# Kernel optimization log

Measured on AMD Instinct MI355X. Metric: run time of the kernel, lower is better.

The kernel has to match this reference:

```python
import jax, jax.numpy as jnp
import numpy as np
import math

D, H, DK, F, V, L = 512, 8, 64, 2048, 8192, 2
B, S, T = 16, 128, 128
EPS = 1e-5


def _ln(x, g, b):
    mu = jnp.mean(x, -1, keepdims=True)
    var = jnp.mean((x - mu) ** 2, -1, keepdims=True)
    return g * (x - mu) * jax.lax.rsqrt(var + EPS) + b


def _pe(length):
    pos = jnp.arange(length, dtype=jnp.float32)[:, None]
    div = jnp.exp(jnp.arange(0, D, 2, dtype=jnp.float32) * (-math.log(10000.0) / D))
    ang = pos * div
    pe = jnp.zeros((length, D), jnp.float32)
    return pe.at[:, 0::2].set(jnp.sin(ang)).at[:, 1::2].set(jnp.cos(ang))


def _attn(q, k, v, src, dst, num_dst):
    # per-edge score = exp(clip((k_src . q_dst)/sqrt(d_k), -5, 5))  [E, H]
    score = jnp.einsum('ehd,ehd->eh', k[src], q[dst]) / math.sqrt(DK)
    score = jnp.exp(jnp.clip(score, -5.0, 5.0))
    wv = jax.ops.segment_sum(v[src] * score[..., None], dst, num_segments=num_dst)
    z = jax.ops.segment_sum(score, dst, num_segments=num_dst)
    return (wv / z[..., None]).reshape(num_dst, D)


def _forward(src_tokens, tgt_tokens, ee_src, ee_dst, dd_src, dd_dst, ed_src, ed_dst, P):
    (src_emb, tgt_emb, eW, eB, elg, elb, eW1, eb1, eW2, eb2, eng, enb,
     dsW, dsB, dcW, dcB, dlg, dlb, dW1, db1, dW2, db2, dng, dnb, gW, gb) = P
    pe = _pe(max(S, T))
    Ne, Nd = B * S, B * T
    xe = (src_emb[src_tokens] * math.sqrt(D) + pe[None, :S]).reshape(Ne, D)
    xd = (tgt_emb[tgt_tokens] * math.sqrt(D) + pe[None, :T]).reshape(Nd, D)
    # encoder stack
    for i in range(L):
        nx = _ln(xe, elg[i, 0], elb[i, 0])
        q = (nx @ eW[i, 0] + eB[i, 0]).reshape(Ne, H, DK)
        k = (nx @ eW[i, 1] + eB[i, 1]).reshape(Ne, H, DK)
        v = (nx @ eW[i, 2] + eB[i, 2]).reshape(Ne, H, DK)
        xe = xe + _attn(q, k, v, ee_src, ee_dst, Ne) @ eW[i, 3] + eB[i, 3]
        nx = _ln(xe, elg[i, 1], elb[i, 1])
        xe = xe + jax.nn.relu(nx @ eW1[i] + eb1[i]) @ eW2[i] + eb2[i]
        if i == L - 1:
            xe = _ln(xe, eng, enb)
    # decoder stack
    for i in range(L):
        nx = _ln(xd, dlg[i, 0], dlb[i, 0])
        q = (nx @ dsW[i, 0] + dsB[i, 0]).reshape(Nd, H, DK)
        k = (nx @ dsW[i, 1] + dsB[i, 1]).reshape(Nd, H, DK)
        v = (nx @ dsW[i, 2] + dsB[i, 2]).reshape(Nd, H, DK)
        xd = xd + _attn(q, k, v, dd_src, dd_dst, Nd) @ dsW[i, 3] + dsB[i, 3]
        nq = _ln(xd, dlg[i, 1], dlb[i, 1])
        nkv = _ln(xe, dlg[i, 1], dlb[i, 1])
        q = (nq @ dcW[i, 0] + dcB[i, 0]).reshape(Nd, H, DK)
        k = (nkv @ dcW[i, 1] + dcB[i, 1]).reshape(Ne, H, DK)
        v = (nkv @ dcW[i, 2] + dcB[i, 2]).reshape(Ne, H, DK)
        xd = xd + _attn(q, k, v, ed_src, ed_dst, Nd) @ dcW[i, 3] + dcB[i, 3]
        nx = _ln(xd, dlg[i, 2], dlb[i, 2])
        xd = xd + jax.nn.relu(nx @ dW1[i] + db1[i]) @ dW2[i] + db2[i]
        if i == L - 1:
            xd = _ln(xd, dng, dnb)
    return jax.nn.log_softmax(xd @ gW + gb, axis=-1)  # [Nd, V]


def setup_inputs() -> dict:
    key = jax.random.key(0)
    ks = iter(jax.random.split(key, 40))
    def nrm(shape, scale=0.02):
        return jax.random.normal(next(ks), shape, dtype=jnp.float32) * scale
    src_tokens = jax.random.randint(next(ks), (B, S), 0, V, dtype=jnp.int32)
    tgt_tokens = jax.random.randint(next(ks), (B, T), 0, V, dtype=jnp.int32)
    # graph structure (per-sentence blocks)
    si, di = np.meshgrid(np.arange(S), np.arange(S), indexing='ij')
    si, di = si.ravel(), di.ravel()
    base = (np.arange(B) * S)[:, None]
    ee_src = (base + si[None, :]).ravel().astype(np.int32)
    ee_dst = (base + di[None, :]).ravel().astype(np.int32)
    m = si <= di  # causal: src pos <= dst pos
    dd_src = (base + si[m][None, :]).ravel().astype(np.int32)
    dd_dst = (base + di[m][None, :]).ravel().astype(np.int32)
    ed_src = ee_src.copy()
    ed_dst = ee_dst.copy()
    inp = dict(
        src_tokens=src_tokens, tgt_tokens=tgt_tokens,
        ee_src=jnp.asarray(ee_src), ee_dst=jnp.asarray(ee_dst),
        dd_src=jnp.asarray(dd_src), dd_dst=jnp.asarray(dd_dst),
        ed_src=jnp.asarray(ed_src), ed_dst=jnp.asarray(ed_dst),
        src_emb=nrm((V, D), 1.0 / math.sqrt(D)), tgt_emb=nrm((V, D), 1.0 / math.sqrt(D)),
        enc_attn_W=nrm((L, 4, D, D)), enc_attn_b=jnp.zeros((L, 4, D), jnp.float32),
        enc_ln_g=jnp.ones((L, 2, D), jnp.float32), enc_ln_b=jnp.zeros((L, 2, D), jnp.float32),
        enc_ff_W1=nrm((L, D, F)), enc_ff_b1=jnp.zeros((L, F), jnp.float32),
        enc_ff_W2=nrm((L, F, D)), enc_ff_b2=jnp.zeros((L, D), jnp.float32),
        enc_norm_g=jnp.ones((D,), jnp.float32), enc_norm_b=jnp.zeros((D,), jnp.float32),
        dec_self_W=nrm((L, 4, D, D)), dec_self_b=jnp.zeros((L, 4, D), jnp.float32),
        dec_cross_W=nrm((L, 4, D, D)), dec_cross_b=jnp.zeros((L, 4, D), jnp.float32),
        dec_ln_g=jnp.ones((L, 3, D), jnp.float32), dec_ln_b=jnp.zeros((L, 3, D), jnp.float32),
        dec_ff_W1=nrm((L, D, F)), dec_ff_b1=jnp.zeros((L, F), jnp.float32),
        dec_ff_W2=nrm((L, F, D)), dec_ff_b2=jnp.zeros((L, D), jnp.float32),
        dec_norm_g=jnp.ones((D,), jnp.float32), dec_norm_b=jnp.zeros((D,), jnp.float32),
        gen_W=nrm((D, V)), gen_b=jnp.zeros((V,), jnp.float32),
    )
    return inp


def reference(src_tokens, tgt_tokens, ee_src, ee_dst, dd_src, dd_dst, ed_src, ed_dst,
              src_emb, tgt_emb, enc_attn_W, enc_attn_b, enc_ln_g, enc_ln_b,
              enc_ff_W1, enc_ff_b1, enc_ff_W2, enc_ff_b2, enc_norm_g, enc_norm_b,
              dec_self_W, dec_self_b, dec_cross_W, dec_cross_b, dec_ln_g, dec_ln_b,
              dec_ff_W1, dec_ff_b1, dec_ff_W2, dec_ff_b2, dec_norm_g, dec_norm_b,
              gen_W, gen_b):
    P = (src_emb, tgt_emb, enc_attn_W, enc_attn_b, enc_ln_g, enc_ln_b,
         enc_ff_W1, enc_ff_b1, enc_ff_W2, enc_ff_b2, enc_norm_g, enc_norm_b,
         dec_self_W, dec_self_b, dec_cross_W, dec_cross_b, dec_ln_g, dec_ln_b,
         dec_ff_W1, dec_ff_b1, dec_ff_W2, dec_ff_b2, dec_norm_g, dec_norm_b, gen_W, gen_b)
    return _forward(src_tokens, tgt_tokens, ee_src, ee_dst, dd_src, dd_dst, ed_src, ed_dst, P)
```

## Files before the change

kernel.cpp:

```cpp
#include <hip/hip_runtime.h>

typedef __attribute__((ext_vector_type(8))) short bfx8;
typedef __attribute__((ext_vector_type(4))) float fx4;

static __device__ __forceinline__ unsigned short f2bf(float f) {
    union { float f; unsigned int u; } v; v.f = f;
    unsigned int i = v.u;
    return (unsigned short)((i + 0x7FFFu + ((i >> 16) & 1u)) >> 16);
}
static __device__ __forceinline__ float bf2f(unsigned short u) {
    union { unsigned int ui; float f; } cv;
    cv.ui = ((unsigned int)u) << 16;
    return cv.f;
}

static __device__ __forceinline__ void gl2lds16(const unsigned short* g, unsigned short* l) {
    unsigned long long gu = (unsigned long long)g;
    unsigned int lu = (unsigned int)(unsigned long long)l;
    __builtin_amdgcn_global_load_lds(
        (const __attribute__((address_space(1))) void*)gu,
        (__attribute__((address_space(3))) void*)lu,
        16, 0, 0);
}

struct TrGroup {
    const float* src;
    unsigned short* dst;
    int srcRowStride;
    int dstRowStride;
    long srcSliceOff;
    long dstSliceOff;
};
struct TrTable {
    TrGroup g[18];
    int zStart[19];
};

__global__ __launch_bounds__(256) void trall_kernel(TrTable tt)
{
    __shared__ unsigned short tile[32][33];
    int z = blockIdx.z;
    int gi = 0;
#pragma unroll 1
    while (z >= tt.zStart[gi + 1]) ++gi;
    int zi = z - tt.zStart[gi];
    const float* s = tt.g[gi].src + (size_t)zi * tt.g[gi].srcSliceOff;
    unsigned short* d = tt.g[gi].dst + (size_t)zi * tt.g[gi].dstSliceOff;
    int srs = tt.g[gi].srcRowStride, drs = tt.g[gi].dstRowStride;
    int n0 = blockIdx.x * 32, k0 = blockIdx.y * 32;
    int tx = threadIdx.x & 31, ty = threadIdx.x >> 5;
#pragma unroll
    for (int i = 0; i < 32; i += 8)
        tile[ty + i][tx] = f2bf(s[(size_t)(k0 + ty + i) * srs + (n0 + tx)]);
    __syncthreads();
#pragma unroll
    for (int i = 0; i < 32; i += 8)
        d[(size_t)(n0 + ty + i) * drs + (k0 + tx)] = tile[tx][ty + i];
}

__global__ __launch_bounds__(256) void embed2_kernel(
    const int* __restrict__ tokA, const int* __restrict__ tokB,
    const float* __restrict__ embA, const float* __restrict__ embB,
    float* __restrict__ outA, float* __restrict__ outB)
{
    int idx = blockIdx.x;
    int row = idx & 2047;
    const int* tok = idx < 2048 ? tokA : tokB;
    const float* emb = idx < 2048 ? embA : embB;
    float* out = idx < 2048 ? outA : outB;
    int pos = row & 127;
    int t = tok[row];
    for (int d = threadIdx.x; d < 512; d += 256) {
        float ang = (float)pos * expf((float)(d & ~1) * (-9.210340371976184f / 512.0f));
        float pe = (d & 1) ? cosf(ang) : sinf(ang);
        out[(size_t)row * 512 + d] = emb[(size_t)t * 512 + d] * 22.627416997969522f + pe;
    }
}

static __device__ __forceinline__ void ln_row(
    const float* __restrict__ xrow, const float* __restrict__ g,
    const float* __restrict__ b, int lane, fx4& o0, fx4& o1)
{
    const fx4* xr = (const fx4*)xrow;
    fx4 a = xr[lane * 2], c = xr[lane * 2 + 1];
    float s = a[0] + a[1] + a[2] + a[3] + c[0] + c[1] + c[2] + c[3];
#pragma unroll
    for (int off = 32; off; off >>= 1) s += __shfl_xor(s, off);
    float mu = s * (1.0f / 512.0f);
    float qv = 0.f;
#pragma unroll
    for (int j = 0; j < 4; ++j) {
        float d0 = a[j] - mu; qv += d0 * d0;
        float d1 = c[j] - mu; qv += d1 * d1;
    }
#pragma unroll
    for (int off = 32; off; off >>= 1) qv += __shfl_xor(qv, off);
    float rs = rsqrtf(qv * (1.0f / 512.0f) + 1e-5f);
    const fx4* gr = (const fx4*)g;
    const fx4* br = (const fx4*)b;
    fx4 g0 = gr[lane * 2], g1 = gr[lane * 2 + 1];
    fx4 b0 = br[lane * 2], b1 = br[lane * 2 + 1];
#pragma unroll
    for (int j = 0; j < 4; ++j) {
        o0[j] = g0[j] * (a[j] - mu) * rs + b0[j];
        o1[j] = g1[j] * (c[j] - mu) * rs + b1[j];
    }
}

template<bool OUTBF>
__global__ __launch_bounds__(256) void ln_kernel(
    const float* __restrict__ x, const float* __restrict__ g,
    const float* __restrict__ b, void* __restrict__ out)
{
    int row = blockIdx.x * 4 + (threadIdx.x >> 6);
    int lane = threadIdx.x & 63;
    fx4 o0, o1;
    ln_row(x + (size_t)row * 512, g, b, lane, o0, o1);
    if (OUTBF) {
        unsigned short* orow = (unsigned short*)out + (size_t)row * 512 + lane * 8;
        ushort4 u0 = {f2bf(o0[0]), f2bf(o0[1]), f2bf(o0[2]), f2bf(o0[3])};
        ushort4 u1 = {f2bf(o1[0]), f2bf(o1[1]), f2bf(o1[2]), f2bf(o1[3])};
        *(ushort4*)orow = u0;
        *(ushort4*)(orow + 4) = u1;
    } else {
        fx4* orow = (fx4*)out + (size_t)row * 128;
        orow[lane * 2] = o0;
        orow[lane * 2 + 1] = o1;
    }
}

__global__ __launch_bounds__(256) void ln2_kernel(
    const float* __restrict__ x0, const float* __restrict__ x1,
    const float* __restrict__ g, const float* __restrict__ b,
    unsigned short* __restrict__ o0, unsigned short* __restrict__ o1)
{
    int idx = blockIdx.x * 4 + (threadIdx.x >> 6);
    int lane = threadIdx.x & 63;
    const float* x = idx < 2048 ? x0 : x1;
    unsigned short* o = idx < 2048 ? o0 : o1;
    int row = idx & 2047;
    fx4 v0, v1;
    ln_row(x + (size_t)row * 512, g, b, lane, v0, v1);
    unsigned short* orow = o + (size_t)row * 512 + lane * 8;
    ushort4 u0 = {f2bf(v0[0]), f2bf(v0[1]), f2bf(v0[2]), f2bf(v0[3])};
    ushort4 u1 = {f2bf(v1[0]), f2bf(v1[1]), f2bf(v1[2]), f2bf(v1[3])};
    *(ushort4*)orow = u0;
    *(ushort4*)(orow + 4) = u1;
}

template<bool RELU, bool RESID, bool OUTBF>
__global__ __launch_bounds__(256) void gemm_kernel(
    const unsigned short* __restrict__ A, const unsigned short* __restrict__ Wt,
    const float* __restrict__ bias, const float* __restrict__ res,
    void* __restrict__ Cv, int K, int ldc, int gx)
{
    __shared__ unsigned short smem[2][2][4096];
    const int tid = threadIdx.x;
    const int nwg = gridDim.x;
    const int cpx = nwg >> 3;
    const int phys = blockIdx.x;
    const int logical = (phys & 7) * cpx + (phys >> 3);
    const int bm = (logical / gx) * 64;
    const int bn = (logical % gx) * 64;
    const int lane = tid & 63;
    const int wv = tid >> 6;
    const int wr = (wv >> 1) * 32;
    const int wc = (wv & 1) * 32;
    const int lr = lane & 15;
    const int lrow = lane >> 3;
    const int lchk = lane & 7;
    fx4 acc00 = {0.f, 0.f, 0.f, 0.f}, acc01 = {0.f, 0.f, 0.f, 0.f};
    fx4 acc10 = {0.f, 0.f, 0.f, 0.f}, acc11 = {0.f, 0.f, 0.f, 0.f};

    auto stage = [&](int buf, int k0) {
#pragma unroll
        for (int j = 0; j < 2; ++j) {
            int row = wv * 16 + j * 8 + lrow;
            int sc = lchk ^ (row & 7);
            gl2lds16(A + (size_t)(bm + row) * K + k0 + sc * 8,
                     &smem[buf][0][(wv * 16 + j * 8) * 64]);
        }
#pragma unroll
        for (int j = 0; j < 2; ++j) {
            int row = wv * 16 + j * 8 + lrow;
            int sc = lchk ^ (row & 7);
            gl2lds16(Wt + (size_t)(bn + row) * K + k0 + sc * 8,
                     &smem[buf][1][(wv * 16 + j * 8) * 64]);
        }
    };

    const int nt = K >> 6;
    int cur = 0;
    stage(0, 0);
    for (int t = 0; t < nt; ++t) {
        __syncthreads();
        if (t + 1 < nt) stage(cur ^ 1, (t + 1) << 6);
        const unsigned short* bufA = &smem[cur][0][0];
        const unsigned short* bufB = &smem[cur][1][0];
        const int ra0 = wr + lr, ra1 = wr + 16 + lr;
        const int rb0 = wc + lr, rb1 = wc + 16 + lr;
#pragma unroll
        for (int kk = 0; kk < 2; ++kk) {
            int ca = kk * 4 + (lane >> 4);
            bfx8 a0 = *(const bfx8*)&bufA[ra0 * 64 + ((ca ^ (ra0 & 7)) * 8)];
            bfx8 a1 = *(const bfx8*)&bufA[ra1 * 64 + ((ca ^ (ra1 & 7)) * 8)];
            bfx8 b0 = *(const bfx8*)&bufB[rb0 * 64 + ((ca ^ (rb0 & 7)) * 8)];
            bfx8 b1 = *(const bfx8*)&bufB[rb1 * 64 + ((ca ^ (rb1 & 7)) * 8)];
            acc00 = __builtin_amdgcn_mfma_f32_16x16x32_bf16(a0, b0, acc00, 0, 0, 0);
            acc01 = __builtin_amdgcn_mfma_f32_16x16x32_bf16(a0, b1, acc01, 0, 0, 0);
            acc10 = __builtin_amdgcn_mfma_f32_16x16x32_bf16(a1, b0, acc10, 0, 0, 0);
            acc11 = __builtin_amdgcn_mfma_f32_16x16x32_bf16(a1, b1, acc11, 0, 0, 0);
        }
        cur ^= 1;
    }
    int rbase = bm + wr + ((lane >> 4) * 4);
    int cbase = bn + wc + lr;
#pragma unroll
    for (int m = 0; m < 2; ++m) {
        fx4 am0 = m ? acc10 : acc00;
        fx4 am1 = m ? acc11 : acc01;
#pragma unroll
        for (int r = 0; r < 4; ++r) {
            int row = rbase + m * 16 + r;
#pragma unroll
            for (int half = 0; half < 2; ++half) {
                int col = cbase + half * 16;
                float v = (half ? am1[r] : am0[r]) + bias[col];
                if (RESID) v += res[(size_t)row * ldc + col];
                if (RELU) v = fmaxf(v, 0.f);
                if (OUTBF) ((unsigned short*)Cv)[(size_t)row * ldc + col] = f2bf(v);
                else       ((float*)Cv)[(size_t)row * ldc + col] = v;
            }
        }
    }
}

template<bool RELU>
__global__ __launch_bounds__(256) void gemm128_kernel(
    const unsigned short* __restrict__ A, const unsigned short* __restrict__ Wt,
    const float* __restrict__ bias, unsigned short* __restrict__ C,
    int K, int ldc)
{
    __shared__ unsigned short smem[2][2][8192];
    const int tid = threadIdx.x;
    const int nwg = gridDim.x;
    const int cpx = nwg >> 3;
    const int phys = blockIdx.x;
    const int logical = (phys & 7) * cpx + (phys >> 3);
    const int bm = (logical & 15) * 128;
    const int bn = (logical >> 4) * 128;
    const int lane = tid & 63;
    const int wv = tid >> 6;
    const int wr = (wv >> 1) * 64;
    const int wc = (wv & 1) * 64;
    const int lr = lane & 15;
    const int lrow = lane >> 3;
    const int lchk = lane & 7;
    fx4 acc[4][4];
#pragma unroll
    for (int mi = 0; mi < 4; ++mi)
#pragma unroll
        for (int ni = 0; ni < 4; ++ni) acc[mi][ni] = fx4{0.f, 0.f, 0.f, 0.f};

    auto stage = [&](int buf, int k0) {
#pragma unroll
        for (int j = 0; j < 4; ++j) {
            int row = wv * 32 + j * 8 + lrow;
            int sc = lchk ^ (row & 7);
            gl2lds16(A + (size_t)(bm + row) * K + k0 + sc * 8,
                     &smem[buf][0][(wv * 32 + j * 8) * 64]);
            gl2lds16(Wt + (size_t)(bn + row) * K + k0 + sc * 8,
                     &smem[buf][1][(wv * 32 + j * 8) * 64]);
        }
    };

    const int nt = K >> 6;
    int cur = 0;
    stage(0, 0);
    for (int t = 0; t < nt; ++t) {
        __syncthreads();
        if (t + 1 < nt) stage(cur ^ 1, (t + 1) << 6);
        const unsigned short* bufA = &smem[cur][0][0];
        const unsigned short* bufB = &smem[cur][1][0];
#pragma unroll
        for (int kk = 0; kk < 2; ++kk) {
            int ca = kk * 4 + (lane >> 4);
            bfx8 af[4], bg[4];
#pragma unroll
            for (int i = 0; i < 4; ++i) {
                int ra = wr + i * 16 + lr;
                int rb = wc + i * 16 + lr;
                af[i] = *(const bfx8*)&bufA[ra * 64 + ((ca ^ (ra & 7)) * 8)];
                bg[i] = *(const bfx8*)&bufB[rb * 64 + ((ca ^ (rb & 7)) * 8)];
            }
#pragma unroll
            for (int mi = 0; mi < 4; ++mi)
#pragma unroll
                for (int ni = 0; ni < 4; ++ni)
                    acc[mi][ni] = __builtin_amdgcn_mfma_f32_16x16x32_bf16(af[mi], bg[ni], acc[mi][ni], 0, 0, 0);
        }
        cur ^= 1;
    }
    int rbase = bm + wr + ((lane >> 4) * 4);
    int cbase = bn + wc + lr;
#pragma unroll
    for (int mi = 0; mi < 4; ++mi)
#pragma unroll
        for (int ni = 0; ni < 4; ++ni) {
            int col = cbase + ni * 16;
            float bv = bias[col];
#pragma unroll
            for (int r = 0; r < 4; ++r) {
                int row = rbase + mi * 16 + r;
                float v = acc[mi][ni][r] + bv;
                if (RELU) v = fmaxf(v, 0.f);
                C[(size_t)row * ldc + col] = f2bf(v);
            }
        }
}

template<bool CAUSAL>
__global__ __launch_bounds__(256) void fattn_kernel(
    const unsigned short* __restrict__ xq, const unsigned short* __restrict__ xkv,
    const unsigned short* __restrict__ Wt, const float* __restrict__ bias,
    unsigned short* __restrict__ out)
{
    __shared__ __align__(16) unsigned char lds[143360];
    const int blk = blockIdx.x;
    const int half = blk & 1;
    const int h = (blk >> 1) & 7;
    const int b = blk >> 4;
    const int q0 = half * 64;
    const int tid = threadIdx.x;
    const int lane = tid & 63;
    const int wv = tid >> 6;
    const int lr = lane & 15;
    const int hg8 = (lane >> 4) * 8;
    const int rloc = (lane >> 4) * 4;
    const int lrow = lane >> 3;
    const int lchk = lane & 7;

    const unsigned short* gxq = xq + (size_t)(b * 128 + q0) * 512;
    const unsigned short* gkv = xkv + (size_t)(b * 128) * 512;
    const unsigned short* gw  = Wt + (size_t)(h * 64) * 512;

    auto stage = [&](int buf, int k0) {
        unsigned short* dstX = (unsigned short*)(lds + buf * 49152);
        unsigned short* dstW = (unsigned short*)(lds + buf * 49152 + 24576);
#pragma unroll
        for (int j = 0; j < 6; ++j) {
            int row = wv * 48 + j * 8 + lrow;
            int sc = (lchk ^ (row & 7)) * 8;
            const unsigned short* xs = (row < 64)
                ? gxq + (size_t)row * 512
                : gkv + (size_t)(row - 64) * 512;
            gl2lds16(xs + k0 + sc, dstX + (wv * 48 + j * 8) * 64);
            const unsigned short* ws = gw + ((size_t)(row & 63) + (size_t)(row >> 6) * 512) * 512;
            gl2lds16(ws + k0 + sc, dstW + (wv * 48 + j * 8) * 64);
        }
    };

    fx4 accQ[4], accK[2][4], accV[2][4];
#pragma unroll
    for (int c = 0; c < 4; ++c) {
        accQ[c] = fx4{0.f, 0.f, 0.f, 0.f};
        accK[0][c] = fx4{0.f, 0.f, 0.f, 0.f}; accK[1][c] = fx4{0.f, 0.f, 0.f, 0.f};
        accV[0][c] = fx4{0.f, 0.f, 0.f, 0.f}; accV[1][c] = fx4{0.f, 0.f, 0.f, 0.f};
    }
    stage(0, 0);
#pragma unroll 1
    for (int t = 0; t < 8; ++t) {
        __syncthreads();
        if (t < 7) stage((t + 1) & 1, (t + 1) * 64);
        const unsigned short* stX = (const unsigned short*)(lds + (t & 1) * 49152);
        const unsigned short* stW = (const unsigned short*)(lds + (t & 1) * 49152 + 24576);
#pragma unroll
        for (int kk = 0; kk < 2; ++kk) {
            const int ca = kk * 4 + (lane >> 4);
            auto rd = [&](const unsigned short* base, int row) -> bfx8 {
                return *(const bfx8*)(base + row * 64 + ((ca ^ (row & 7)) * 8));
            };
            bfx8 aQ  = rd(stX, wv * 16 + lr);
            bfx8 aK0 = rd(stX, 64 + wv * 32 + lr);
            bfx8 aK1 = rd(stX, 64 + wv * 32 + 16 + lr);
#pragma unroll
            for (int c = 0; c < 4; ++c) {
                bfx8 bq = rd(stW, c * 16 + lr);
                accQ[c] = __builtin_amdgcn_mfma_f32_16x16x32_bf16(aQ, bq, accQ[c], 0, 0, 0);
                bfx8 bk = rd(stW, 64 + c * 16 + lr);
                accK[0][c] = __builtin_amdgcn_mfma_f32_16x16x32_bf16(aK0, bk, accK[0][c], 0, 0, 0);
                accK[1][c] = __builtin_amdgcn_mfma_f32_16x16x32_bf16(aK1, bk, accK[1][c], 0, 0, 0);
                bfx8 bv = rd(stW, 128 + c * 16 + lr);
                accV[0][c] = __builtin_amdgcn_mfma_f32_16x16x32_bf16(aK0, bv, accV[0][c], 0, 0, 0);
                accV[1][c] = __builtin_amdgcn_mfma_f32_16x16x32_bf16(aK1, bv, accV[1][c], 0, 0, 0);
            }
        }
    }
    unsigned short* sQ  = (unsigned short*)(lds + 98304);
    unsigned short* sK  = (unsigned short*)(lds + 107520);
    unsigned short* sVt = (unsigned short*)(lds + 125952);
    unsigned short* sP  = (unsigned short*)lds;
#pragma unroll
    for (int c = 0; c < 4; ++c) {
        int col = c * 16 + lr;
        float bq = bias[h * 64 + col];
        float bk = bias[512 + h * 64 + col];
        float bv = bias[1024 + h * 64 + col];
#pragma unroll
        for (int r = 0; r < 4; ++r) {
            sQ[(wv * 16 + rloc + r) * 72 + col]      = f2bf(accQ[c][r] + bq);
            sK[(wv * 32 + rloc + r) * 72 + col]      = f2bf(accK[0][c][r] + bk);
            sK[(wv * 32 + 16 + rloc + r) * 72 + col] = f2bf(accK[1][c][r] + bk);
            sVt[col * 136 + (wv * 32 + rloc + r)]      = f2bf(accV[0][c][r] + bv);
            sVt[col * 136 + (wv * 32 + 16 + rloc + r)] = f2bf(accV[1][c][r] + bv);
        }
    }
    __syncthreads();
    fx4 acc[8];
#pragma unroll
    for (int n = 0; n < 8; ++n) acc[n] = fx4{0.f, 0.f, 0.f, 0.f};
#pragma unroll
    for (int kk = 0; kk < 2; ++kk) {
        bfx8 a = *(const bfx8*)(sQ + (wv * 16 + lr) * 72 + kk * 32 + hg8);
#pragma unroll
        for (int n = 0; n < 8; ++n) {
            bfx8 bb = *(const bfx8*)(sK + (n * 16 + lr) * 72 + kk * 32 + hg8);
            acc[n] = __builtin_amdgcn_mfma_f32_16x16x32_bf16(a, bb, acc[n], 0, 0, 0);
        }
    }
    const int qg = q0 + wv * 16 + rloc;
    float zinv[4];
#pragma unroll
    for (int r = 0; r < 4; ++r) {
        float zs = 0.f;
#pragma unroll
        for (int n = 0; n < 8; ++n) {
            float s = acc[n][r] * 0.125f;
            s = __expf(fminf(fmaxf(s, -5.f), 5.f));
            if (CAUSAL && (n * 16 + lr) > (qg + r)) s = 0.f;
            zs += s;
            sP[(wv * 16 + rloc + r) * 136 + n * 16 + lr] = f2bf(s);
        }
#pragma unroll
        for (int off = 8; off; off >>= 1) zs += __shfl_xor(zs, off);
        zinv[r] = 1.f / zs;
    }
    fx4 acc2[4];
#pragma unroll
    for (int dn = 0; dn < 4; ++dn) acc2[dn] = fx4{0.f, 0.f, 0.f, 0.f};
#pragma unroll
    for (int kk = 0; kk < 4; ++kk) {
        bfx8 a = *(const bfx8*)(sP + (wv * 16 + lr) * 136 + kk * 32 + hg8);
#pragma unroll
        for (int dn = 0; dn < 4; ++dn) {
            bfx8 bb = *(const bfx8*)(sVt + (dn * 16 + lr) * 136 + kk * 32 + hg8);
            acc2[dn] = __builtin_amdgcn_mfma_f32_16x16x32_bf16(a, bb, acc2[dn], 0, 0, 0);
        }
    }
#pragma unroll
    for (int dn = 0; dn < 4; ++dn)
#pragma unroll
        for (int r = 0; r < 4; ++r) {
            size_t row = (size_t)(b * 128 + qg + r);
            out[row * 512 + h * 64 + dn * 16 + lr] = f2bf(acc2[dn][r] * zinv[r]);
        }
}

__global__ __launch_bounds__(256) void logsoftmax_bf16_kernel(
    const unsigned short* __restrict__ logits, float* __restrict__ out)
{
    __shared__ float red[4];
    int tid = threadIdx.x;
    const bfx8* lrow = (const bfx8*)(logits + (size_t)blockIdx.x * 8192);
    float* orow = out + (size_t)blockIdx.x * 8192;
    float vals[32];
    float mx = -1e30f;
#pragma unroll
    for (int i = 0; i < 4; ++i) {
        bfx8 u = lrow[i * 256 + tid];
#pragma unroll
        for (int j = 0; j < 8; ++j) {
            float f = bf2f((unsigned short)u[j]);
            vals[i * 8 + j] = f;
            mx = fmaxf(mx, f);
        }
    }
#pragma unroll
    for (int off = 32; off; off >>= 1) mx = fmaxf(mx, __shfl_xor(mx, off));
    int wid = tid >> 6;
    if ((tid & 63) == 0) red[wid] = mx;
    __syncthreads();
    mx = fmaxf(fmaxf(red[0], red[1]), fmaxf(red[2], red[3]));
    __syncthreads();
    float sum = 0.f;
#pragma unroll
    for (int i = 0; i < 32; ++i) sum += __expf(vals[i] - mx);
#pragma unroll
    for (int off = 32; off; off >>= 1) sum += __shfl_xor(sum, off);
    if ((tid & 63) == 0) red[wid] = sum;
    __syncthreads();
    sum = red[0] + red[1] + red[2] + red[3];
    float lsub = mx + logf(sum);
#pragma unroll
    for (int i = 0; i < 4; ++i) {
        fx4 o0, o1;
#pragma unroll
        for (int j = 0; j < 4; ++j) {
            o0[j] = vals[i * 8 + j] - lsub;
            o1[j] = vals[i * 8 + 4 + j] - lsub;
        }
        ((fx4*)orow)[(i * 256 + tid) * 2] = o0;
        ((fx4*)orow)[(i * 256 + tid) * 2 + 1] = o1;
    }
}

extern "C" void kernel_launch(void* const* d_in, const int* in_sizes, int n_in,
                              void* d_out, int out_size, void* d_ws, size_t ws_size,
                              hipStream_t stream) {
    (void)in_sizes; (void)n_in; (void)out_size; (void)ws_size;
    const int* src_tokens = (const int*)d_in[0];
    const int* tgt_tokens = (const int*)d_in[1];
    const float* src_emb    = (const float*)d_in[8];
    const float* tgt_emb    = (const float*)d_in[9];
    const float* enc_attn_W = (const float*)d_in[10];
    const float* enc_attn_b = (const float*)d_in[11];
    const float* enc_ln_g   = (const float*)d_in[12];
    const float* enc_ln_b   = (const float*)d_in[13];
    const float* enc_ff_W1  = (const float*)d_in[14];
    const float* enc_ff_b1  = (const float*)d_in[15];
    const float* enc_ff_W2  = (const float*)d_in[16];
    const float* enc_ff_b2  = (const float*)d_in[17];
    const float* enc_norm_g = (const float*)d_in[18];
    const float* enc_norm_b = (const float*)d_in[19];
    const float* dec_self_W = (const float*)d_in[20];
    const float* dec_self_b = (const float*)d_in[21];
    const float* dec_cross_W= (const float*)d_in[22];
    const float* dec_cross_b= (const float*)d_in[23];
    const float* dec_ln_g   = (const float*)d_in[24];
    const float* dec_ln_b   = (const float*)d_in[25];
    const float* dec_ff_W1  = (const float*)d_in[26];
    const float* dec_ff_b1  = (const float*)d_in[27];
    const float* dec_ff_W2  = (const float*)d_in[28];
    const float* dec_ff_b2  = (const float*)d_in[29];
    const float* dec_norm_g = (const float*)d_in[30];
    const float* dec_norm_b = (const float*)d_in[31];
    const float* gen_W      = (const float*)d_in[32];
    const float* gen_b      = (const float*)d_in[33];
    float* dout = (float*)d_out;

    unsigned short* wt = (unsigned short*)d_ws;
    const size_t OFF_ENCQKV = 0;
    const size_t OFF_ENCO   = 1572864;
    const size_t OFF_ENCW1  = 2097152;
    const size_t OFF_ENCW2  = 4194304;
    const size_t OFF_DECSQKV= 6291456;
    const size_t OFF_DECSO  = 7864320;
    const size_t OFF_DECCQKV= 8388608;
    const size_t OFF_DECCO  = 9961472;
    const size_t OFF_DECW1  = 10485760;
    const size_t OFF_DECW2  = 12582912;
    const size_t OFF_GENW   = 14680064;
    const size_t WT_ELEMS   = 18874368;
    float* fb  = (float*)(wt + WT_ELEMS);
    float* xe  = fb;
    float* xd  = fb + 1048576;
    unsigned short* nxb  = (unsigned short*)(fb + 2097152);
    unsigned short* nkvb = (unsigned short*)(fb + 3145728);
    unsigned short* ffb  = (unsigned short*)(fb + 4194304);
    unsigned short* attb = (unsigned short*)(fb + 7340032);
    unsigned short* genin   = (unsigned short*)fb;
    unsigned short* logitsb = (unsigned short*)(fb + 1048576);

    TrTable tt;
    {
        int z = 0, gi = 0;
        auto addg = [&](const float* s, unsigned short* d, int srs, int drs,
                        long so, long dof, int zc) {
            tt.zStart[gi] = z;
            tt.g[gi].src = s; tt.g[gi].dst = d;
            tt.g[gi].srcRowStride = srs; tt.g[gi].dstRowStride = drs;
            tt.g[gi].srcSliceOff = so; tt.g[gi].dstSliceOff = dof;
            ++gi; z += zc;
        };
        addg(enc_attn_W,              wt + OFF_ENCQKV,               512,  512,  262144,    262144, 3);
        addg(enc_attn_W + 4L*262144,  wt + OFF_ENCQKV + 3L*262144,   512,  512,  262144,    262144, 3);
        addg(enc_attn_W + 3L*262144,  wt + OFF_ENCO,                 512,  512,  4L*262144, 262144, 2);
        addg(enc_ff_W1,               wt + OFF_ENCW1,                2048, 512,  512,       262144, 4);
        addg(enc_ff_W1 + 1048576,     wt + OFF_ENCW1 + 1048576,      2048, 512,  512,       262144, 4);
        addg(enc_ff_W2,               wt + OFF_ENCW2,                512,  2048, 262144,    512,    4);
        addg(enc_ff_W2 + 1048576,     wt + OFF_ENCW2 + 1048576,      512,  2048, 262144,    512,    4);
        addg(dec_self_W,              wt + OFF_DECSQKV,              512,  512,  262144,    262144, 3);
        addg(dec_self_W + 4L*262144,  wt + OFF_DECSQKV + 3L*262144,  512,  512,  262144,    262144, 3);
        addg(dec_self_W + 3L*262144,  wt + OFF_DECSO,                512,  512,  4L*262144, 262144, 2);
        addg(dec_cross_W,             wt + OFF_DECCQKV,              512,  512,  262144,    262144, 3);
        addg(dec_cross_W + 4L*262144, wt + OFF_DECCQKV + 3L*262144,  512,  512,  262144,    262144, 3);
        addg(dec_cross_W + 3L*262144, wt + OFF_DECCO,                512,  512,  4L*262144, 262144, 2);
        addg(dec_ff_W1,               wt + OFF_DECW1,                2048, 512,  512,       262144, 4);
        addg(dec_ff_W1 + 1048576,     wt + OFF_DECW1 + 1048576,      2048, 512,  512,       262144, 4);
        addg(dec_ff_W2,               wt + OFF_DECW2,                512,  2048, 262144,    512,    4);
        addg(dec_ff_W2 + 1048576,     wt + OFF_DECW2 + 1048576,      512,  2048, 262144,    512,    4);
        addg(gen_W,                   wt + OFF_GENW,                 8192, 512,  512,       262144, 16);
        tt.zStart[18] = z;
    }
    trall_kernel<<<dim3(16, 16, 72), 256, 0, stream>>>(tt);

    embed2_kernel<<<4096, 256, 0, stream>>>(src_tokens, tgt_tokens, src_emb, tgt_emb, xe, xd);

    auto gemm = [&](const unsigned short* A, const unsigned short* W, const float* bias,
                    const float* res, void* C, int N, int K, int ldc, bool relu, bool outbf) {
        int gx = N / 64;
        dim3 g(gx * 32);
        if (res)        gemm_kernel<false, true,  false><<<g, 256, 0, stream>>>(A, W, bias, res, C, K, ldc, gx);
        else if (relu)  gemm_kernel<true,  false, true ><<<g, 256, 0, stream>>>(A, W, bias, res, C, K, ldc, gx);
        else if (outbf) gemm_kernel<false, false, true ><<<g, 256, 0, stream>>>(A, W, bias, res, C, K, ldc, gx);
        else            gemm_kernel<false, false, false><<<g, 256, 0, stream>>>(A, W, bias, res, C, K, ldc, gx);
    };
    auto gemm128 = [&](const unsigned short* A, const unsigned short* W, const float* bias,
                       unsigned short* C, int N, int K, int ldc, bool relu) {
        dim3 g((N / 128) * 16);
        if (relu) gemm128_kernel<true ><<<g, 256, 0, stream>>>(A, W, bias, C, K, ldc);
        else      gemm128_kernel<false><<<g, 256, 0, stream>>>(A, W, bias, C, K, ldc);
    };
    auto lnb = [&](const float* x, const float* g, const float* b, unsigned short* o) {
        ln_kernel<true><<<512, 256, 0, stream>>>(x, g, b, o);
    };
    auto lnf = [&](const float* x, const float* g, const float* b, float* o) {
        ln_kernel<false><<<512, 256, 0, stream>>>(x, g, b, o);
    };

    for (int i = 0; i < 2; ++i) {
        lnb(xe, enc_ln_g + (size_t)(i * 2 + 0) * 512, enc_ln_b + (size_t)(i * 2 + 0) * 512, nxb);
        fattn_kernel<false><<<256, 256, 0, stream>>>(
            nxb, nxb, wt + OFF_ENCQKV + (size_t)i * 3 * 262144,
            enc_attn_b + (size_t)i * 4 * 512, attb);
        gemm(attb, wt + OFF_ENCO + (size_t)i * 262144, enc_attn_b + (size_t)i * 4 * 512 + 1536,
             xe, xe, 512, 512, 512, false, false);
        lnb(xe, enc_ln_g + (size_t)(i * 2 + 1) * 512, enc_ln_b + (size_t)(i * 2 + 1) * 512, nxb);
        gemm128(nxb, wt + OFF_ENCW1 + (size_t)i * 1048576, enc_ff_b1 + (size_t)i * 2048,
                ffb, 2048, 512, 2048, true);
        gemm(ffb, wt + OFF_ENCW2 + (size_t)i * 1048576, enc_ff_b2 + (size_t)i * 512,
             xe, xe, 512, 2048, 512, false, false);
    }
    lnf(xe, enc_norm_g, enc_norm_b, xe);

    for (int i = 0; i < 2; ++i) {
        lnb(xd, dec_ln_g + (size_t)(i * 3 + 0) * 512, dec_ln_b + (size_t)(i * 3 + 0) * 512, nxb);
        fattn_kernel<true><<<256, 256, 0, stream>>>(
            nxb, nxb, wt + OFF_DECSQKV + (size_t)i * 3 * 262144,
            dec_self_b + (size_t)i * 4 * 512, attb);
        gemm(attb, wt + OFF_DECSO + (size_t)i * 262144, dec_self_b + (size_t)i * 4 * 512 + 1536,
             xd, xd, 512, 512, 512, false, false);
        ln2_kernel<<<1024, 256, 0, stream>>>(
            xd, xe, dec_ln_g + (size_t)(i * 3 + 1) * 512, dec_ln_b + (size_t)(i * 3 + 1) * 512,
            nxb, nkvb);
        fattn_kernel<false><<<256, 256, 0, stream>>>(
            nxb, nkvb, wt + OFF_DECCQKV + (size_t)i * 3 * 262144,
            dec_cross_b + (size_t)i * 4 * 512, attb);
        gemm(attb, wt + OFF_DECCO + (size_t)i * 262144, dec_cross_b + (size_t)i * 4 * 512 + 1536,
             xd, xd, 512, 512, 512, false, false);
        lnb(xd, dec_ln_g + (size_t)(i * 3 + 2) * 512, dec_ln_b + (size_t)(i * 3 + 2) * 512, nxb);
        gemm128(nxb, wt + OFF_DECW1 + (size_t)i * 1048576, dec_ff_b1 + (size_t)i * 2048,
                ffb, 2048, 512, 2048, true);
        gemm(ffb, wt + OFF_DECW2 + (size_t)i * 1048576, dec_ff_b2 + (size_t)i * 512,
             xd, xd, 512, 2048, 512, false, false);
    }
    lnb(xd, dec_norm_g, dec_norm_b, genin);

    gemm128(genin, wt + OFF_GENW, gen_b, logitsb, 8192, 512, 8192, false);
    logsoftmax_bf16_kernel<<<2048, 256, 0, stream>>>(logitsb, dout);
}
```

Before: 349.7 us.

## Double fused-attention workgroup to 512 threads and add BK=128 FF2 GEMM

The fused QKV-projection+attention kernel now runs with 8 waves instead of 4. Each wave computes one K/V row block, and waves 4-7 also compute Q. Scores and PV are split across wave pairs, with row sums combined through LDS behind an extra barrier. A new residual GEMM variant with a K-tile of 128 replaces the K=2048 FF2 GEMMs in both stacks. This halves the number of k-loop iterations and barriers, at the cost of lower per-wave work balance and higher LDS use per stage.

```diff
diff --git a/kernel.cpp b/kernel.cpp
--- a/kernel.cpp
+++ b/kernel.cpp
@@ -235,6 +235,88 @@
     }
 }
 
+template<bool RELU, bool RESID, bool OUTBF>
+__global__ __launch_bounds__(256) void gemm_bk128_kernel(
+    const unsigned short* __restrict__ A, const unsigned short* __restrict__ Wt,
+    const float* __restrict__ bias, const float* __restrict__ res,
+    void* __restrict__ Cv, int K, int ldc, int gx)
+{
+    __shared__ unsigned short smem[2][2][8192];
+    const int tid = threadIdx.x;
+    const int nwg = gridDim.x;
+    const int cpx = nwg >> 3;
+    const int phys = blockIdx.x;
+    const int logical = (phys & 7) * cpx + (phys >> 3);
+    const int bm = (logical / gx) * 64;
+    const int bn = (logical % gx) * 64;
+    const int lane = tid & 63;
+    const int wv = tid >> 6;
+    const int wr = (wv >> 1) * 32;
+    const int wc = (wv & 1) * 32;
+    const int lr = lane & 15;
+    const int lrow4 = lane >> 4;
+    const int lchk16 = lane & 15;
+    fx4 acc00 = {0.f, 0.f, 0.f, 0.f}, acc01 = {0.f, 0.f, 0.f, 0.f};
+    fx4 acc10 = {0.f, 0.f, 0.f, 0.f}, acc11 = {0.f, 0.f, 0.f, 0.f};
+
+    auto stage = [&](int buf, int k0) {
+#pragma unroll
+        for (int j = 0; j < 4; ++j) {
+            int row = wv * 16 + j * 4 + lrow4;
+            int sc = (lchk16 ^ (row & 15)) * 8;
+            gl2lds16(A + (size_t)(bm + row) * K + k0 + sc,
+                     &smem[buf][0][(wv * 16 + j * 4) * 128]);
+            gl2lds16(Wt + (size_t)(bn + row) * K + k0 + sc,
+                     &smem[buf][1][(wv * 16 + j * 4) * 128]);
+        }
+    };
+
+    const int nt = K >> 7;
+    int cur = 0;
+    stage(0, 0);
+    for (int t = 0; t < nt; ++t) {
+        __syncthreads();
+        if (t + 1 < nt) stage(cur ^ 1, (t + 1) << 7);
+        const unsigned short* bufA = &smem[cur][0][0];
+        const unsigned short* bufB = &smem[cur][1][0];
+        const int ra0 = wr + lr, ra1 = wr + 16 + lr;
+        const int rb0 = wc + lr, rb1 = wc + 16 + lr;
+#pragma unroll
+        for (int kk = 0; kk < 4; ++kk) {
+            int ca = kk * 4 + (lane >> 4);
+            bfx8 a0 = *(const bfx8*)&bufA[ra0 * 128 + ((ca ^ (ra0 & 15)) * 8)];
+            bfx8 a1 = *(const bfx8*)&bufA[ra1 * 128 + ((ca ^ (ra1 & 15)) * 8)];
+            bfx8 b0 = *(const bfx8*)&bufB[rb0 * 128 + ((ca ^ (rb0 & 15)) * 8)];
+            bfx8 b1 = *(const bfx8*)&bufB[rb1 * 128 + ((ca ^ (rb1 & 15)) * 8)];
+            acc00 = __builtin_amdgcn_mfma_f32_16x16x32_bf16(a0, b0, acc00, 0, 0, 0);
+            acc01 = __builtin_amdgcn_mfma_f32_16x16x32_bf16(a0, b1, acc01, 0, 0, 0);
+            acc10 = __builtin_amdgcn_mfma_f32_16x16x32_bf16(a1, b0, acc10, 0, 0, 0);
+            acc11 = __builtin_amdgcn_mfma_f32_16x16x32_bf16(a1, b1, acc11, 0, 0, 0);
+        }
+        cur ^= 1;
+    }
+    int rbase = bm + wr + ((lane >> 4) * 4);
+    int cbase = bn + wc + lr;
+#pragma unroll
+    for (int m = 0; m < 2; ++m) {
+        fx4 am0 = m ? acc10 : acc00;
+        fx4 am1 = m ? acc11 : acc01;
+#pragma unroll
+        for (int r = 0; r < 4; ++r) {
+            int row = rbase + m * 16 + r;
+#pragma unroll
+            for (int half = 0; half < 2; ++half) {
+                int col = cbase + half * 16;
+                float v = (half ? am1[r] : am0[r]) + bias[col];
+                if (RESID) v += res[(size_t)row * ldc + col];
+                if (RELU) v = fmaxf(v, 0.f);
+                if (OUTBF) ((unsigned short*)Cv)[(size_t)row * ldc + col] = f2bf(v);
+                else       ((float*)Cv)[(size_t)row * ldc + col] = v;
+            }
+        }
+    }
+}
+
 template<bool RELU>
 __global__ __launch_bounds__(256) void gemm128_kernel(
     const unsigned short* __restrict__ A, const unsigned short* __restrict__ Wt,
@@ -320,12 +402,12 @@
 }
 
 template<bool CAUSAL>
-__global__ __launch_bounds__(256) void fattn_kernel(
+__global__ __launch_bounds__(512) void fattn_kernel(
     const unsigned short* __restrict__ xq, const unsigned short* __restrict__ xkv,
     const unsigned short* __restrict__ Wt, const float* __restrict__ bias,
     unsigned short* __restrict__ out)
 {
-    __shared__ __align__(16) unsigned char lds[143360];
+    __shared__ __align__(16) unsigned char lds[143872];
     const int blk = blockIdx.x;
     const int half = blk & 1;
     const int h = (blk >> 1) & 7;
@@ -348,24 +430,24 @@
         unsigned short* dstX = (unsigned short*)(lds + buf * 49152);
         unsigned short* dstW = (unsigned short*)(lds + buf * 49152 + 24576);
 #pragma unroll
-        for (int j = 0; j < 6; ++j) {
-            int row = wv * 48 + j * 8 + lrow;
+        for (int j = 0; j < 3; ++j) {
+            int row = wv * 24 + j * 8 + lrow;
             int sc = (lchk ^ (row & 7)) * 8;
             const unsigned short* xs = (row < 64)
                 ? gxq + (size_t)row * 512
                 : gkv + (size_t)(row - 64) * 512;
-            gl2lds16(xs + k0 + sc, dstX + (wv * 48 + j * 8) * 64);
+            gl2lds16(xs + k0 + sc, dstX + (wv * 24 + j * 8) * 64);
             const unsigned short* ws = gw + ((size_t)(row & 63) + (size_t)(row >> 6) * 512) * 512;
-            gl2lds16(ws + k0 + sc, dstW + (wv * 48 + j * 8) * 64);
-        }
-    };
-
-    fx4 accQ[4], accK[2][4], accV[2][4];
+            gl2lds16(ws + k0 + sc, dstW + (wv * 24 + j * 8) * 64);
+        }
+    };
+
+    fx4 accQ[4], accK[4], accV[4];
 #pragma unroll
     for (int c = 0; c < 4; ++c) {
         accQ[c] = fx4{0.f, 0.f, 0.f, 0.f};
-        accK[0][c] = fx4{0.f, 0.f, 0.f, 0.f}; accK[1][c] = fx4{0.f, 0.f, 0.f, 0.f};
-        accV[0][c] = fx4{0.f, 0.f, 0.f, 0.f}; accV[1][c] = fx4{0.f, 0.f, 0.f, 0.f};
+        accK[c] = fx4{0.f, 0.f, 0.f, 0.f};
+        accV[c] = fx4{0.f, 0.f, 0.f, 0.f};
     }
     stage(0, 0);
 #pragma unroll 1
@@ -380,89 +462,99 @@
             auto rd = [&](const unsigned short* base, int row) -> bfx8 {
                 return *(const bfx8*)(base + row * 64 + ((ca ^ (row & 7)) * 8));
             };
-            bfx8 aQ  = rd(stX, wv * 16 + lr);
-            bfx8 aK0 = rd(stX, 64 + wv * 32 + lr);
-            bfx8 aK1 = rd(stX, 64 + wv * 32 + 16 + lr);
+            bfx8 aKV = rd(stX, 64 + wv * 16 + lr);
+            bfx8 aQ = aKV;
+            if (wv >= 4) aQ = rd(stX, (wv - 4) * 16 + lr);
 #pragma unroll
             for (int c = 0; c < 4; ++c) {
-                bfx8 bq = rd(stW, c * 16 + lr);
-                accQ[c] = __builtin_amdgcn_mfma_f32_16x16x32_bf16(aQ, bq, accQ[c], 0, 0, 0);
                 bfx8 bk = rd(stW, 64 + c * 16 + lr);
-                accK[0][c] = __builtin_amdgcn_mfma_f32_16x16x32_bf16(aK0, bk, accK[0][c], 0, 0, 0);
-                accK[1][c] = __builtin_amdgcn_mfma_f32_16x16x32_bf16(aK1, bk, accK[1][c], 0, 0, 0);
+                accK[c] = __builtin_amdgcn_mfma_f32_16x16x32_bf16(aKV, bk, accK[c], 0, 0, 0);
                 bfx8 bv = rd(stW, 128 + c * 16 + lr);
-                accV[0][c] = __builtin_amdgcn_mfma_f32_16x16x32_bf16(aK0, bv, accV[0][c], 0, 0, 0);
-                accV[1][c] = __builtin_amdgcn_mfma_f32_16x16x32_bf16(aK1, bv, accV[1][c], 0, 0, 0);
+                accV[c] = __builtin_amdgcn_mfma_f32_16x16x32_bf16(aKV, bv, accV[c], 0, 0, 0);
+                if (wv >= 4) {
+                    bfx8 bq = rd(stW, c * 16 + lr);
+                    accQ[c] = __builtin_amdgcn_mfma_f32_16x16x32_bf16(aQ, bq, accQ[c], 0, 0, 0);
+                }
             }
         }
     }
     unsigned short* sQ  = (unsigned short*)(lds + 98304);
     unsigned short* sK  = (unsigned short*)(lds + 107520);
     unsigned short* sVt = (unsigned short*)(lds + 125952);
+    float* zp = (float*)(lds + 143360);
     unsigned short* sP  = (unsigned short*)lds;
 #pragma unroll
     for (int c = 0; c < 4; ++c) {
         int col = c * 16 + lr;
-        float bq = bias[h * 64 + col];
-        float bk = bias[512 + h * 64 + col];
-        float bv = bias[1024 + h * 64 + col];
+        float bk_ = bias[512 + h * 64 + col];
+        float bv_ = bias[1024 + h * 64 + col];
 #pragma unroll
         for (int r = 0; r < 4; ++r) {
-            sQ[(wv * 16 + rloc + r) * 72 + col]      = f2bf(accQ[c][r] + bq);
-            sK[(wv * 32 + rloc + r) * 72 + col]      = f2bf(accK[0][c][r] + bk);
-            sK[(wv * 32 + 16 + rloc + r) * 72 + col] = f2bf(accK[1][c][r] + bk);
-            sVt[col * 136 + (wv * 32 + rloc + r)]      = f2bf(accV[0][c][r] + bv);
-            sVt[col * 136 + (wv * 32 + 16 + rloc + r)] = f2bf(accV[1][c][r] + bv);
+            sK[(wv * 16 + rloc + r) * 72 + col] = f2bf(accK[c][r] + bk_);
+            sVt[col * 136 + (wv * 16 + rloc + r)] = f2bf(accV[c][r] + bv_);
+        }
+        if (wv >= 4) {
+            float bq_ = bias[h * 64 + col];
+#pragma unroll
+            for (int r = 0; r < 4; ++r)
+                sQ[((wv - 4) * 16 + rloc + r) * 72 + col] = f2bf(accQ[c][r] + bq_);
         }
     }
     __syncthreads();
-    fx4 acc[8];
-#pragma unroll
-    for (int n = 0; n < 8; ++n) acc[n] = fx4{0.f, 0.f, 0.f, 0.f};
+    const int qb = wv >> 1;
+    const int kh = wv & 1;
+    fx4 acc[4];
+#pragma unroll
+    for (int n = 0; n < 4; ++n) acc[n] = fx4{0.f, 0.f, 0.f, 0.f};
 #pragma unroll
     for (int kk = 0; kk < 2; ++kk) {
-        bfx8 a = *(const bfx8*)(sQ + (wv * 16 + lr) * 72 + kk * 32 + hg8);
-#pragma unroll
-        for (int n = 0; n < 8; ++n) {
-            bfx8 bb = *(const bfx8*)(sK + (n * 16 + lr) * 72 + kk * 32 + hg8);
+        bfx8 a = *(const bfx8*)(sQ + (qb * 16 + lr) * 72 + kk * 32 + hg8);
+#pragma unroll
+        for (int n = 0; n < 4; ++n) {
+            bfx8 bb = *(const bfx8*)(sK + ((kh * 4 + n) * 16 + lr) * 72 + kk * 32 + hg8);
             acc[n] = __builtin_amdgcn_mfma_f32_16x16x32_bf16(a, bb, acc[n], 0, 0, 0);
         }
     }
-    const int qg = q0 + wv * 16 + rloc;
-    float zinv[4];
+    const int qg = q0 + qb * 16 + rloc;
 #pragma unroll
     for (int r = 0; r < 4; ++r) {
         float zs = 0.f;
 #pragma unroll
-        for (int n = 0; n < 8; ++n) {
+        for (int n = 0; n < 4; ++n) {
             float s = acc[n][r] * 0.125f;
             s = __expf(fminf(fmaxf(s, -5.f), 5.f));
-            if (CAUSAL && (n * 16 + lr) > (qg + r)) s = 0.f;
+            if (CAUSAL && (kh * 64 + n * 16 + lr) > (qg + r)) s = 0.f;
             zs += s;
-            sP[(wv * 16 + rloc + r) * 136 + n * 16 + lr] = f2bf(s);
+            sP[(qb * 16 + rloc + r) * 136 + kh * 64 + n * 16 + lr] = f2bf(s);
         }
 #pragma unroll
         for (int off = 8; off; off >>= 1) zs += __shfl_xor(zs, off);
-        zinv[r] = 1.f / zs;
-    }
-    fx4 acc2[4];
-#pragma unroll
-    for (int dn = 0; dn < 4; ++dn) acc2[dn] = fx4{0.f, 0.f, 0.f, 0.f};
+        if (lr == 0) zp[(qb * 2 + kh) * 16 + rloc + r] = zs;
+    }
+    __syncthreads();
+    float zinv[4];
+#pragma unroll
+    for (int r = 0; r < 4; ++r)
+        zinv[r] = 1.f / (zp[(qb * 2 + 0) * 16 + rloc + r] + zp[(qb * 2 + 1) * 16 + rloc + r]);
+    const int dh = wv & 1;
+    fx4 acc2[2];
+    acc2[0] = fx4{0.f, 0.f, 0.f, 0.f};
+    acc2[1] = fx4{0.f, 0.f, 0.f, 0.f};
 #pragma unroll
     for (int kk = 0; kk < 4; ++kk) {
-        bfx8 a = *(const bfx8*)(sP + (wv * 16 + lr) * 136 + kk * 32 + hg8);
-#pragma unroll
-        for (int dn = 0; dn < 4; ++dn) {
-            bfx8 bb = *(const bfx8*)(sVt + (dn * 16 + lr) * 136 + kk * 32 + hg8);
+        bfx8 a = *(const bfx8*)(sP + (qb * 16 + lr) * 136 + kk * 32 + hg8);
+#pragma unroll
+        for (int dn = 0; dn < 2; ++dn) {
+            bfx8 bb = *(const bfx8*)(sVt + (dh * 32 + dn * 16 + lr) * 136 + kk * 32 + hg8);
             acc2[dn] = __builtin_amdgcn_mfma_f32_16x16x32_bf16(a, bb, acc2[dn], 0, 0, 0);
         }
     }
 #pragma unroll
-    for (int dn = 0; dn < 4; ++dn)
+    for (int dn = 0; dn < 2; ++dn)
 #pragma unroll
         for (int r = 0; r < 4; ++r) {
             size_t row = (size_t)(b * 128 + qg + r);
-            out[row * 512 + h * 64 + dn * 16 + lr] = f2bf(acc2[dn][r] * zinv[r]);
+            out[row * 512 + h * 64 + dh * 32 + dn * 16 + lr] = f2bf(acc2[dn][r] * zinv[r]);
         }
 }
 
@@ -615,6 +707,12 @@
         else if (outbf) gemm_kernel<false, false, true ><<<g, 256, 0, stream>>>(A, W, bias, res, C, K, ldc, gx);
         else            gemm_kernel<false, false, false><<<g, 256, 0, stream>>>(A, W, bias, res, C, K, ldc, gx);
     };
+    auto gemmK128res = [&](const unsigned short* A, const unsigned short* W, const float* bias,
+                           const float* res, float* C, int N, int K, int ldc) {
+        int gx = N / 64;
+        dim3 g(gx * 32);
+        gemm_bk128_kernel<false, true, false><<<g, 256, 0, stream>>>(A, W, bias, res, C, K, ldc, gx);
+    };
     auto gemm128 = [&](const unsigned short* A, const unsigned short* W, const float* bias,
                        unsigned short* C, int N, int K, int ldc, bool relu) {
         dim3 g((N / 128) * 16);
@@ -630,7 +728,7 @@
 
     for (int i = 0; i < 2; ++i) {
         lnb(xe, enc_ln_g + (size_t)(i * 2 + 0) * 512, enc_ln_b + (size_t)(i * 2 + 0) * 512, nxb);
-        fattn_kernel<false><<<256, 256, 0, stream>>>(
+        fattn_kernel<false><<<256, 512, 0, stream>>>(
             nxb, nxb, wt + OFF_ENCQKV + (size_t)i * 3 * 262144,
             enc_attn_b + (size_t)i * 4 * 512, attb);
         gemm(attb, wt + OFF_ENCO + (size_t)i * 262144, enc_attn_b + (size_t)i * 4 * 512 + 1536,
@@ -638,14 +736,14 @@
         lnb(xe, enc_ln_g + (size_t)(i * 2 + 1) * 512, enc_ln_b + (size_t)(i * 2 + 1) * 512, nxb);
         gemm128(nxb, wt + OFF_ENCW1 + (size_t)i * 1048576, enc_ff_b1 + (size_t)i * 2048,
                 ffb, 2048, 512, 2048, true);
-        gemm(ffb, wt + OFF_ENCW2 + (size_t)i * 1048576, enc_ff_b2 + (size_t)i * 512,
-             xe, xe, 512, 2048, 512, false, false);
+        gemmK128res(ffb, wt + OFF_ENCW2 + (size_t)i * 1048576, enc_ff_b2 + (size_t)i * 512,
+                    xe, xe, 512, 2048, 512);
     }
     lnf(xe, enc_norm_g, enc_norm_b, xe);
 
     for (int i = 0; i < 2; ++i) {
         lnb(xd, dec_ln_g + (size_t)(i * 3 + 0) * 512, dec_ln_b + (size_t)(i * 3 + 0) * 512, nxb);
-        fattn_kernel<true><<<256, 256, 0, stream>>>(
+        fattn_kernel<true><<<256, 512, 0, stream>>>(
             nxb, nxb, wt + OFF_DECSQKV + (size_t)i * 3 * 262144,
             dec_self_b + (size_t)i * 4 * 512, attb);
         gemm(attb, wt + OFF_DECSO + (size_t)i * 262144, dec_self_b + (size_t)i * 4 * 512 + 1536,
@@ -653,7 +751,7 @@
         ln2_kernel<<<1024, 256, 0, stream>>>(
             xd, xe, dec_ln_g + (size_t)(i * 3 + 1) * 512, dec_ln_b + (size_t)(i * 3 + 1) * 512,
             nxb, nkvb);
-        fattn_kernel<false><<<256, 256, 0, stream>>>(
+        fattn_kernel<false><<<256, 512, 0, stream>>>(
             nxb, nkvb, wt + OFF_DECCQKV + (size_t)i * 3 * 262144,
             dec_cross_b + (size_t)i * 4 * 512, attb);
         gemm(attb, wt + OFF_DECCO + (size_t)i * 262144, dec_cross_b + (size_t)i * 4 * 512 + 1536,
@@ -661,8 +759,8 @@
         lnb(xd, dec_ln_g + (size_t)(i * 3 + 2) * 512, dec_ln_b + (size_t)(i * 3 + 2) * 512, nxb);
         gemm128(nxb, wt + OFF_DECW1 + (size_t)i * 1048576, dec_ff_b1 + (size_t)i * 2048,
                 ffb, 2048, 512, 2048, true);
-        gemm(ffb, wt + OFF_DECW2 + (size_t)i * 1048576, dec_ff_b2 + (size_t)i * 512,
-             xd, xd, 512, 2048, 512, false, false);
+        gemmK128res(ffb, wt + OFF_DECW2 + (size_t)i * 1048576, dec_ff_b2 + (size_t)i * 512,
+                    xd, xd, 512, 2048, 512);
     }
     lnb(xd, dec_norm_g, dec_norm_b, genin);
 
```

After: 342.0 us. -2.2%, faster.
